# Performance work log

Measured on AMD Instinct MI355X. Metric: run time of the kernel, lower is better.

The kernel has to match this reference:

```python
import jax, jax.numpy as jnp
import numpy as np

EMBED_DIM = 256
N_HEADS = 1
NORM_FACTOR = float(np.sqrt(EMBED_DIM / N_HEADS))


def setup_inputs() -> dict:
    key = jax.random.key(0)
    ks = jax.random.split(key, 7)
    B, S, E = 4, 4096, EMBED_DIM
    scale = 1.0 / np.sqrt(E)
    x = jax.random.normal(ks[0], (B, S, E), dtype=jnp.float32)
    Wq = jax.random.normal(ks[1], (E, E), dtype=jnp.float32) * scale
    bq = jax.random.normal(ks[2], (E,), dtype=jnp.float32) * 0.01
    Wk = jax.random.normal(ks[3], (E, E), dtype=jnp.float32) * scale
    bk = jax.random.normal(ks[4], (E,), dtype=jnp.float32) * 0.01
    Wv = jax.random.normal(ks[5], (E, E), dtype=jnp.float32) * scale
    bv = jax.random.normal(ks[6], (E,), dtype=jnp.float32) * 0.01
    return {"x": x, "Wq": Wq, "bq": bq, "Wk": Wk, "bk": bk, "Wv": Wv, "bv": bv}


def reference(x, Wq, bq, Wk, bk, Wv, bv):
    # Linear projections (torch Linear: x @ W.T + b; W here stored as [in, out]-equivalent square)
    q = x @ Wq + bq  # [B, S, E]
    k = x @ Wk + bk  # [B, S, E]
    v = x @ Wv + bv  # [B, S, E]
    # Full attention scores [B, S, S], scaled by sqrt(embed_dim / n_heads)
    attn_scores = jnp.einsum('bse,bte->bst', q, k) / NORM_FACTOR
    attn_dist = jax.nn.softmax(attn_scores, axis=-1)
    pooled = jnp.einsum('bst,bte->bse', attn_dist, v)  # [B, S, E]
    return pooled.mean(axis=1, keepdims=True)  # [B, 1, E]
```

## Files before the change

### kernel.cpp

```cpp
#include <hip/hip_runtime.h>
#include <hip/hip_fp8.h>
#include <stdint.h>

#define SS 4096
#define EE 256
#define C2 0.0901684400555602f
#define SCALE1 0x7F7F7F7F

typedef __bf16 bf16x8 __attribute__((ext_vector_type(8)));
typedef float  f32x4  __attribute__((ext_vector_type(4)));
typedef int    i32x8  __attribute__((ext_vector_type(8)));

#if __has_builtin(__builtin_amdgcn_exp2f)
#define EXP2(x) __builtin_amdgcn_exp2f(x)
#else
#define EXP2(x) exp2f(x)
#endif
#if __has_builtin(__builtin_amdgcn_rcpf)
#define RCP(x) __builtin_amdgcn_rcpf(x)
#else
#define RCP(x) (1.0f / (x))
#endif

__device__ __forceinline__ uint16_t bf16_rn(float f) {
  uint32_t u = __float_as_uint(f);
  uint32_t r = (u + 0x7fffu + ((u >> 16) & 1u)) >> 16;
  return (uint16_t)r;
}
__device__ __forceinline__ float bf2f(uint16_t h) {
  return __uint_as_float(((uint32_t)h) << 16);
}
__device__ __forceinline__ bf16x8 pack_bf8(float4 a, float4 b) {
  union { bf16x8 v; uint16_t u[8]; } r;
  r.u[0] = bf16_rn(a.x); r.u[1] = bf16_rn(a.y);
  r.u[2] = bf16_rn(a.z); r.u[3] = bf16_rn(a.w);
  r.u[4] = bf16_rn(b.x); r.u[5] = bf16_rn(b.y);
  r.u[6] = bf16_rn(b.z); r.u[7] = bf16_rn(b.w);
  return r.v;
}
__device__ __forceinline__ uint8_t f32_to_e4m3(float x) {
#if __has_builtin(__builtin_amdgcn_cvt_pk_fp8_f32)
  return (uint8_t)(__builtin_amdgcn_cvt_pk_fp8_f32(x, 0.f, 0, false) & 0xff);
#else
  __hip_fp8_e4m3 h(x);
  return (uint8_t)h.__x;
#endif
}

__device__ __forceinline__ f32x4 mfma16(bf16x8 a, bf16x8 b, f32x4 c) {
  return __builtin_amdgcn_mfma_f32_16x16x32_bf16(a, b, c, 0, 0, 0);
}
__device__ __forceinline__ f32x4 mfma128(i32x8 a, i32x8 b, f32x4 c) {
  return __builtin_amdgcn_mfma_scale_f32_16x16x128_f8f6f4(
      a, b, c, 0 , 0 , 0, SCALE1, 0, SCALE1);
}

template<int R>
__device__ __forceinline__ void stage_tile(const uint16_t* gsrc, char* lds, int tid) {
  constexpr int NPER = (R * 32) / 256;
  const int wave = tid >> 6;
  #pragma unroll
  for (int c = 0; c < NPER; ++c) {
    int chunk = c * 256 + tid;
    int r = chunk >> 5;
    int ccl = (chunk & 31) ^ (r & 31);
    const char* gp = (const char*)gsrc + (r * 32 + ccl) * 16;
    char* lp = lds + (c * 256 + wave * 64) * 16;
    __builtin_amdgcn_global_load_lds(
        (const __attribute__((address_space(1))) uint32_t*)(uintptr_t)gp,
        (__attribute__((address_space(3))) uint32_t*)(uintptr_t)lp,
        16, 0, 0);
  }
}
__device__ __forceinline__ bf16x8 read_frag(const char* lds, int row, int cc) {
  int ccp = cc ^ (row & 31);
  return *(const bf16x8*)(lds + (row * 32 + ccp) * 16);
}

__device__ __forceinline__ void stage_fp8_64(const uint8_t* gsrc, char* lds, int tid) {
  #pragma unroll
  for (int c = 0; c < 4; ++c) {
    int chunk = c * 256 + tid;
    int r = chunk >> 4;
    int ccl = (chunk & 15) ^ (r & 15);
    const char* gp = (const char*)gsrc + (r * 16 + ccl) * 16;
    char* lp = lds + (c * 256 + (tid >> 6) * 64) * 16;
    __builtin_amdgcn_global_load_lds(
        (const __attribute__((address_space(1))) uint32_t*)(uintptr_t)gp,
        (__attribute__((address_space(3))) uint32_t*)(uintptr_t)lp,
        16, 0, 0);
  }
}
__device__ __forceinline__ i32x8 read_frag8(const char* lds, int t, int win, int quad) {
  union { i32x8 v; uint4 q[2]; } r;
  int cc0 = win * 8 + quad * 2;
  r.q[0] = *(const uint4*)(lds + (t * 16 + ((cc0 + 0) ^ (t & 15))) * 16);
  r.q[1] = *(const uint4*)(lds + (t * 16 + ((cc0 + 1) ^ (t & 15))) * 16);
  return r.v;
}

__global__ void prep_kernel(const float* __restrict__ Wq, const float* __restrict__ Wk,
                            const float* __restrict__ Wv, uint16_t* __restrict__ wt,
                            float* __restrict__ zbase, float* __restrict__ out) {
  __shared__ float t[64][65];
  const int bid = blockIdx.x, tid = threadIdx.x;
  if (bid >= 48) {
    int idx = (bid - 48) * 256 + tid;
    float4 z = {0.f, 0.f, 0.f, 0.f};
    if (idx < 8192) ((float4*)zbase)[idx] = z;
    else ((float4*)out)[idx - 8192] = z;
    return;
  }
  const int mat = bid >> 4, tt = bid & 15;
  const int ib = (tt >> 2) * 64, ob = (tt & 3) * 64;
  const float* W = (mat == 0) ? Wq : (mat == 1) ? Wk : Wv;
  #pragma unroll
  for (int p = 0; p < 4; ++p) {
    int idx = p * 256 + tid;
    int r = idx >> 4, c4 = idx & 15;
    float4 f = *(const float4*)&W[(size_t)(ib + r) * 256 + ob + c4 * 4];
    t[r][c4 * 4 + 0] = f.x; t[r][c4 * 4 + 1] = f.y;
    t[r][c4 * 4 + 2] = f.z; t[r][c4 * 4 + 3] = f.w;
  }
  __syncthreads();
  #pragma unroll
  for (int p = 0; p < 4; ++p) {
    int idx = p * 256 + tid;
    int o = idx >> 4, i4 = idx & 15;
    ushort4 u;
    u.x = bf16_rn(t[i4 * 4 + 0][o]);
    u.y = bf16_rn(t[i4 * 4 + 1][o]);
    u.z = bf16_rn(t[i4 * 4 + 2][o]);
    u.w = bf16_rn(t[i4 * 4 + 3][o]);
    *(ushort4*)&wt[((size_t)mat * 256 + ob + o) * 256 + ib + i4 * 4] = u;
  }
}

__global__ __launch_bounds__(256, 2) void qkv_kernel(
    const float* __restrict__ x, const uint16_t* __restrict__ wt,
    const float* __restrict__ bq, const float* __restrict__ bk, const float* __restrict__ bv,
    uint8_t* __restrict__ q8, uint8_t* __restrict__ k8, uint16_t* __restrict__ vo) {
  __shared__ char wsm[2][32768];
  const int tid = threadIdx.x;
  const int lane = tid & 63, wave = tid >> 6, quad = lane >> 4, lr = lane & 15;
  const int m0 = (blockIdx.x >> 2) * 128;
  const int cchunk = blockIdx.x & 3;
  stage_tile<64>(wt + (size_t)(cchunk * 192) * 256, wsm[0], tid);
  const float* ab = x + (size_t)(m0 + wave * 32) * EE;
  bf16x8 a[2][8];
  #pragma unroll
  for (int ms = 0; ms < 2; ++ms)
    #pragma unroll
    for (int f = 0; f < 8; ++f) {
      const float* rp = ab + (size_t)(ms * 16 + lr) * EE + f * 32 + quad * 8;
      a[ms][f] = pack_bf8(*(const float4*)rp, *(const float4*)(rp + 4));
    }
  for (int nc = 0; nc < 3; ++nc) {
    __syncthreads();
    if (nc < 2)
      stage_tile<64>(wt + (size_t)(cchunk * 192 + (nc + 1) * 64) * 256, wsm[(nc + 1) & 1], tid);
    const char* tile = wsm[nc & 1];
    #pragma unroll
    for (int nt = 0; nt < 4; ++nt) {
      const int eg0 = cchunk * 192 + nc * 64 + nt * 16;
      const int mat = eg0 >> 8;
      const int e = (eg0 & 255) + lr;
      const float* bias = (mat == 0) ? bq : (mat == 1) ? bk : bv;
      bf16x8 bf[8];
      #pragma unroll
      for (int f = 0; f < 8; ++f) bf[f] = read_frag(tile, nt * 16 + lr, f * 4 + quad);
      f32x4 acc[2] = {};
      #pragma unroll
      for (int f = 0; f < 8; ++f)
        #pragma unroll
        for (int ms = 0; ms < 2; ++ms)
          acc[ms] = mfma16(a[ms][f], bf[f], acc[ms]);
      const float bsv = bias[e];
      #pragma unroll
      for (int ms = 0; ms < 2; ++ms)
        #pragma unroll
        for (int r = 0; r < 4; ++r) {
          int row = m0 + wave * 32 + ms * 16 + quad * 4 + r;
          float vl = acc[ms][r] + bsv;
          if (mat == 2)      vo[(size_t)row * EE + e] = bf16_rn(vl);
          else if (mat == 1) k8[(size_t)row * EE + e] = f32_to_e4m3(vl);
          else               q8[(size_t)row * EE + e] = f32_to_e4m3(vl);
        }
    }
  }
}

__global__ __launch_bounds__(256, 3) void scores_l_kernel(
    const uint8_t* __restrict__ q8, const uint8_t* __restrict__ k8,
    float* __restrict__ lacc) {
  __shared__ char kt[2][16384];
  const int tid = threadIdx.x;
  const int lane = tid & 63, wave = tid >> 6, quad = lane >> 4, lr = lane & 15;
  const int idx = blockIdx.x;
  const int b = idx >> 8, rem = idx & 255, qblk = rem >> 4, kch = rem & 15;
  const uint8_t* qb = q8 + (size_t)(b * SS + qblk * 256 + wave * 64) * EE;
  const uint8_t* kb = k8 + (size_t)(b * SS + kch * 256) * EE;
  stage_fp8_64(kb, kt[0], tid);
  i32x8 a[4][2];
  #pragma unroll
  for (int ms = 0; ms < 4; ++ms)
    #pragma unroll
    for (int win = 0; win < 2; ++win)
      a[ms][win] = *(const i32x8*)(qb + (size_t)(ms * 16 + lr) * EE + win * 128 + quad * 32);
  float accl[16];
  #pragma unroll
  for (int i = 0; i < 16; ++i) accl[i] = 0.f;
  for (int it = 0; it < 4; ++it) {
    __syncthreads();
    if (it + 1 < 4) stage_fp8_64(kb + (size_t)(it + 1) * 64 * EE, kt[(it + 1) & 1], tid);
    const char* tile = kt[it & 1];
    #pragma unroll
    for (int nt = 0; nt < 4; ++nt) {
      i32x8 bf0 = read_frag8(tile, nt * 16 + lr, 0, quad);
      i32x8 bf1 = read_frag8(tile, nt * 16 + lr, 1, quad);
      f32x4 acc[4] = {};
      #pragma unroll
      for (int ms = 0; ms < 4; ++ms) {
        acc[ms] = mfma128(a[ms][0], bf0, acc[ms]);
        acc[ms] = mfma128(a[ms][1], bf1, acc[ms]);
      }
      #pragma unroll
      for (int ms = 0; ms < 4; ++ms)
        #pragma unroll
        for (int r = 0; r < 4; ++r)
          accl[ms * 4 + r] += EXP2(acc[ms][r] * C2);
    }
  }
  #pragma unroll
  for (int d = 1; d < 16; d <<= 1)
    #pragma unroll
    for (int i = 0; i < 16; ++i)
      accl[i] += __shfl_xor(accl[i], d, 64);
  if (lr == 0) {
    float* lp = lacc + b * SS + qblk * 256 + wave * 64;
    #pragma unroll
    for (int ms = 0; ms < 4; ++ms)
      #pragma unroll
      for (int r = 0; r < 4; ++r)
        atomicAdd(&lp[ms * 16 + quad * 4 + r], accl[ms * 4 + r]);
  }
}

__global__ __launch_bounds__(256, 3) void scores_w_kernel(
    const uint8_t* __restrict__ q8, const uint8_t* __restrict__ k8,
    const float* __restrict__ lacc, float* __restrict__ wacc) {
  __shared__ char qt[2][16384];
  __shared__ float rls[256];
  const int tid = threadIdx.x;
  const int lane = tid & 63, wave = tid >> 6, quad = lane >> 4, lr = lane & 15;
  const int idx = blockIdx.x;
  const int b = idx >> 8, rem = idx & 255, kblk = rem >> 4, sch = rem & 15;
  const uint8_t* kb = k8 + (size_t)(b * SS + kblk * 256 + wave * 64) * EE;
  const uint8_t* qw = q8 + (size_t)(b * SS + sch * 256) * EE;
  rls[tid] = lacc[b * SS + sch * 256 + tid];
  stage_fp8_64(qw, qt[0], tid);
  i32x8 a[4][2];
  #pragma unroll
  for (int ms = 0; ms < 4; ++ms)
    #pragma unroll
    for (int win = 0; win < 2; ++win)
      a[ms][win] = *(const i32x8*)(kb + (size_t)(ms * 16 + lr) * EE + win * 128 + quad * 32);
  float accw[16];
  #pragma unroll
  for (int i = 0; i < 16; ++i) accw[i] = 0.f;
  for (int it = 0; it < 4; ++it) {
    __syncthreads();
    if (it + 1 < 4) stage_fp8_64(qw + (size_t)(it + 1) * 64 * EE, qt[(it + 1) & 1], tid);
    const char* tile = qt[it & 1];
    #pragma unroll
    for (int nt = 0; nt < 4; ++nt) {
      float rlv = RCP(rls[it * 64 + nt * 16 + lr]);
      i32x8 bf0 = read_frag8(tile, nt * 16 + lr, 0, quad);
      i32x8 bf1 = read_frag8(tile, nt * 16 + lr, 1, quad);
      f32x4 acc[4] = {};
      #pragma unroll
      for (int ms = 0; ms < 4; ++ms) {
        acc[ms] = mfma128(a[ms][0], bf0, acc[ms]);
        acc[ms] = mfma128(a[ms][1], bf1, acc[ms]);
      }
      #pragma unroll
      for (int ms = 0; ms < 4; ++ms)
        #pragma unroll
        for (int r = 0; r < 4; ++r)
          accw[ms * 4 + r] += EXP2(acc[ms][r] * C2) * rlv;
    }
  }
  #pragma unroll
  for (int d = 1; d < 16; d <<= 1)
    #pragma unroll
    for (int i = 0; i < 16; ++i)
      accw[i] += __shfl_xor(accw[i], d, 64);
  if (lr == 0) {
    float* wp = wacc + b * SS + kblk * 256 + wave * 64;
    #pragma unroll
    for (int ms = 0; ms < 4; ++ms)
      #pragma unroll
      for (int r = 0; r < 4; ++r)
        atomicAdd(&wp[ms * 16 + quad * 4 + r], accw[ms * 4 + r]);
  }
}

__global__ void pool_kernel(const float* __restrict__ wsum, const uint16_t* __restrict__ v,
                            float* __restrict__ out) {
  __shared__ float red[4][256];
  const int b = blockIdx.x >> 6, tc = blockIdx.x & 63;
  const int tq = threadIdx.x >> 6, eg = threadIdx.x & 63;
  float acc[4] = {0.f, 0.f, 0.f, 0.f};
  const float* wp = wsum + b * SS + tc * 64;
  const uint16_t* vp = v + (size_t)(b * SS + tc * 64) * EE + eg * 4;
  #pragma unroll
  for (int t = 0; t < 16; ++t) {
    int row = t * 4 + tq;
    float wv = wp[row];
    ushort4 x4 = *(const ushort4*)(vp + (size_t)row * EE);
    acc[0] += wv * bf2f(x4.x);
    acc[1] += wv * bf2f(x4.y);
    acc[2] += wv * bf2f(x4.z);
    acc[3] += wv * bf2f(x4.w);
  }
  #pragma unroll
  for (int j = 0; j < 4; ++j) red[tq][eg * 4 + j] = acc[j];
  __syncthreads();
  if (tq == 0) {
    const float inv = 1.0f / 4096.0f;
    #pragma unroll
    for (int j = 0; j < 4; ++j) {
      float s = red[0][eg * 4 + j] + red[1][eg * 4 + j] +
                red[2][eg * 4 + j] + red[3][eg * 4 + j];
      atomicAdd(&out[b * 256 + eg * 4 + j], s * inv);
    }
  }
}

extern "C" void kernel_launch(void* const* d_in, const int* in_sizes, int n_in,
                              void* d_out, int out_size, void* d_ws, size_t ws_size,
                              hipStream_t stream) {
  const float* x  = (const float*)d_in[0];
  const float* Wq = (const float*)d_in[1];
  const float* bq = (const float*)d_in[2];
  const float* Wk = (const float*)d_in[3];
  const float* bk = (const float*)d_in[4];
  const float* Wv = (const float*)d_in[5];
  const float* bv = (const float*)d_in[6];

  char* ws = (char*)d_ws;
  uint8_t*  q8   = (uint8_t*)(ws);
  uint8_t*  k8   = (uint8_t*)(ws + 4194304);
  uint16_t* vb   = (uint16_t*)(ws + 8388608);
  uint16_t* wt   = (uint16_t*)(ws + 16777216);
  float* l_arr   = (float*)(ws + 17170432);
  float* w_arr   = (float*)(ws + 17235968);
  float* out     = (float*)d_out;

  prep_kernel<<<81, 256, 0, stream>>>(Wq, Wk, Wv, wt, l_arr, out);
  qkv_kernel<<<512, 256, 0, stream>>>(x, wt, bq, bk, bv, q8, k8, vb);
  scores_l_kernel<<<1024, 256, 0, stream>>>(q8, k8, l_arr);
  scores_w_kernel<<<1024, 256, 0, stream>>>(q8, k8, l_arr, w_arr);
  pool_kernel<<<256, 256, 0, stream>>>(w_arr, vb, out);
}
```

Baseline: 153.7 us.

## Materialize fp8 exp scores once instead of recomputing QK^T in two passes

Replaces the two score passes (one building row sums l, one recomputing QK^T to build column weights) with a single pass. That pass computes exp scores, stores them as an fp8 matrix (64 MB), and accumulates row sums. A new wsum kernel then streams the fp8 matrix, scales each row by 1/l and reduces into per-block partials, which pool_kernel sums. This removes one full fp8 GEMM-plus-exp pass but adds a large HBM write and read, and it clamps exponents at ZMAX, which changes the numerics.

```diff
diff --git a/kernel.cpp b/kernel.cpp
--- a/kernel.cpp
+++ b/kernel.cpp
@@ -6,9 +6,11 @@
 #define EE 256
 #define C2 0.0901684400555602f
 #define SCALE1 0x7F7F7F7F
+#define ZMAX 8.5f
 
 typedef __bf16 bf16x8 __attribute__((ext_vector_type(8)));
 typedef float  f32x4  __attribute__((ext_vector_type(4)));
+typedef float  f32x2  __attribute__((ext_vector_type(2)));
 typedef int    i32x8  __attribute__((ext_vector_type(8)));
 
 #if __has_builtin(__builtin_amdgcn_exp2f)
@@ -44,6 +46,33 @@
 #else
   __hip_fp8_e4m3 h(x);
   return (uint8_t)h.__x;
+#endif
+}
+__device__ __forceinline__ uint32_t pack4_e4m3(float a, float b, float c, float d) {
+#if __has_builtin(__builtin_amdgcn_cvt_pk_fp8_f32)
+  int v = __builtin_amdgcn_cvt_pk_fp8_f32(a, b, 0, false);
+  v = __builtin_amdgcn_cvt_pk_fp8_f32(c, d, v, true);
+  return (uint32_t)v;
+#else
+  return (uint32_t)f32_to_e4m3(a) | ((uint32_t)f32_to_e4m3(b) << 8) |
+         ((uint32_t)f32_to_e4m3(c) << 16) | ((uint32_t)f32_to_e4m3(d) << 24);
+#endif
+}
+__device__ __forceinline__ float e4m3_f32(uint32_t u) {
+  uint32_t bits = ((u & 0x80u) << 24) | ((u & 0x7fu) << 20);
+  return __uint_as_float(bits) * 0x1p+120f;
+}
+__device__ __forceinline__ void decode_fma4(uint32_t w, float rv, float* acc) {
+#if __has_builtin(__builtin_amdgcn_cvt_pk_f32_fp8)
+  f32x2 lo = __builtin_amdgcn_cvt_pk_f32_fp8((int)w, false);
+  f32x2 hi = __builtin_amdgcn_cvt_pk_f32_fp8((int)w, true);
+  acc[0] += rv * lo[0]; acc[1] += rv * lo[1];
+  acc[2] += rv * hi[0]; acc[3] += rv * hi[1];
+#else
+  acc[0] += rv * e4m3_f32(w & 0xffu);
+  acc[1] += rv * e4m3_f32((w >> 8) & 0xffu);
+  acc[2] += rv * e4m3_f32((w >> 16) & 0xffu);
+  acc[3] += rv * e4m3_f32(w >> 24);
 #endif
 }
 
@@ -190,74 +219,18 @@
   }
 }
 
-__global__ __launch_bounds__(256, 3) void scores_l_kernel(
+__global__ __launch_bounds__(256, 3) void scores_pl_kernel(
     const uint8_t* __restrict__ q8, const uint8_t* __restrict__ k8,
-    float* __restrict__ lacc) {
-  __shared__ char kt[2][16384];
-  const int tid = threadIdx.x;
-  const int lane = tid & 63, wave = tid >> 6, quad = lane >> 4, lr = lane & 15;
-  const int idx = blockIdx.x;
-  const int b = idx >> 8, rem = idx & 255, qblk = rem >> 4, kch = rem & 15;
-  const uint8_t* qb = q8 + (size_t)(b * SS + qblk * 256 + wave * 64) * EE;
-  const uint8_t* kb = k8 + (size_t)(b * SS + kch * 256) * EE;
-  stage_fp8_64(kb, kt[0], tid);
-  i32x8 a[4][2];
-  #pragma unroll
-  for (int ms = 0; ms < 4; ++ms)
-    #pragma unroll
-    for (int win = 0; win < 2; ++win)
-      a[ms][win] = *(const i32x8*)(qb + (size_t)(ms * 16 + lr) * EE + win * 128 + quad * 32);
-  float accl[16];
-  #pragma unroll
-  for (int i = 0; i < 16; ++i) accl[i] = 0.f;
-  for (int it = 0; it < 4; ++it) {
-    __syncthreads();
-    if (it + 1 < 4) stage_fp8_64(kb + (size_t)(it + 1) * 64 * EE, kt[(it + 1) & 1], tid);
-    const char* tile = kt[it & 1];
-    #pragma unroll
-    for (int nt = 0; nt < 4; ++nt) {
-      i32x8 bf0 = read_frag8(tile, nt * 16 + lr, 0, quad);
-      i32x8 bf1 = read_frag8(tile, nt * 16 + lr, 1, quad);
-      f32x4 acc[4] = {};
-      #pragma unroll
-      for (int ms = 0; ms < 4; ++ms) {
-        acc[ms] = mfma128(a[ms][0], bf0, acc[ms]);
-        acc[ms] = mfma128(a[ms][1], bf1, acc[ms]);
-      }
-      #pragma unroll
-      for (int ms = 0; ms < 4; ++ms)
-        #pragma unroll
-        for (int r = 0; r < 4; ++r)
-          accl[ms * 4 + r] += EXP2(acc[ms][r] * C2);
-    }
-  }
-  #pragma unroll
-  for (int d = 1; d < 16; d <<= 1)
-    #pragma unroll
-    for (int i = 0; i < 16; ++i)
-      accl[i] += __shfl_xor(accl[i], d, 64);
-  if (lr == 0) {
-    float* lp = lacc + b * SS + qblk * 256 + wave * 64;
-    #pragma unroll
-    for (int ms = 0; ms < 4; ++ms)
-      #pragma unroll
-      for (int r = 0; r < 4; ++r)
-        atomicAdd(&lp[ms * 16 + quad * 4 + r], accl[ms * 4 + r]);
-  }
-}
-
-__global__ __launch_bounds__(256, 3) void scores_w_kernel(
-    const uint8_t* __restrict__ q8, const uint8_t* __restrict__ k8,
-    const float* __restrict__ lacc, float* __restrict__ wacc) {
+    uint8_t* __restrict__ p8, float* __restrict__ lacc) {
   __shared__ char qt[2][16384];
-  __shared__ float rls[256];
+  __shared__ float lsh[256];
   const int tid = threadIdx.x;
   const int lane = tid & 63, wave = tid >> 6, quad = lane >> 4, lr = lane & 15;
   const int idx = blockIdx.x;
   const int b = idx >> 8, rem = idx & 255, kblk = rem >> 4, sch = rem & 15;
   const uint8_t* kb = k8 + (size_t)(b * SS + kblk * 256 + wave * 64) * EE;
   const uint8_t* qw = q8 + (size_t)(b * SS + sch * 256) * EE;
-  rls[tid] = lacc[b * SS + sch * 256 + tid];
+  lsh[tid] = 0.f;
   stage_fp8_64(qw, qt[0], tid);
   i32x8 a[4][2];
   #pragma unroll
@@ -265,16 +238,13 @@
     #pragma unroll
     for (int win = 0; win < 2; ++win)
       a[ms][win] = *(const i32x8*)(kb + (size_t)(ms * 16 + lr) * EE + win * 128 + quad * 32);
-  float accw[16];
-  #pragma unroll
-  for (int i = 0; i < 16; ++i) accw[i] = 0.f;
+  const int tcol0 = kblk * 256 + wave * 64 + quad * 4;
   for (int it = 0; it < 4; ++it) {
     __syncthreads();
     if (it + 1 < 4) stage_fp8_64(qw + (size_t)(it + 1) * 64 * EE, qt[(it + 1) & 1], tid);
     const char* tile = qt[it & 1];
     #pragma unroll
     for (int nt = 0; nt < 4; ++nt) {
-      float rlv = RCP(rls[it * 64 + nt * 16 + lr]);
       i32x8 bf0 = read_frag8(tile, nt * 16 + lr, 0, quad);
       i32x8 bf1 = read_frag8(tile, nt * 16 + lr, 1, quad);
       f32x4 acc[4] = {};
@@ -283,40 +253,79 @@
         acc[ms] = mfma128(a[ms][0], bf0, acc[ms]);
         acc[ms] = mfma128(a[ms][1], bf1, acc[ms]);
       }
-      #pragma unroll
-      for (int ms = 0; ms < 4; ++ms)
-        #pragma unroll
-        for (int r = 0; r < 4; ++r)
-          accw[ms * 4 + r] += EXP2(acc[ms][r] * C2) * rlv;
+      const int sloc = it * 64 + nt * 16 + lr;
+      uint8_t* pr = p8 + (((size_t)(b * SS + sch * 256 + sloc)) << 12) + tcol0;
+      float lpart = 0.f;
+      #pragma unroll
+      for (int ms = 0; ms < 4; ++ms) {
+        float e0 = EXP2(fminf(acc[ms][0] * C2, ZMAX));
+        float e1 = EXP2(fminf(acc[ms][1] * C2, ZMAX));
+        float e2 = EXP2(fminf(acc[ms][2] * C2, ZMAX));
+        float e3 = EXP2(fminf(acc[ms][3] * C2, ZMAX));
+        lpart += (e0 + e1) + (e2 + e3);
+        *(uint32_t*)(pr + ms * 16) = pack4_e4m3(e0, e1, e2, e3);
+      }
+      lpart += __shfl_xor(lpart, 16, 64);
+      lpart += __shfl_xor(lpart, 32, 64);
+      if (quad == 0) atomicAdd(&lsh[sloc], lpart);
     }
   }
-  #pragma unroll
-  for (int d = 1; d < 16; d <<= 1)
-    #pragma unroll
-    for (int i = 0; i < 16; ++i)
-      accw[i] += __shfl_xor(accw[i], d, 64);
-  if (lr == 0) {
-    float* wp = wacc + b * SS + kblk * 256 + wave * 64;
-    #pragma unroll
-    for (int ms = 0; ms < 4; ++ms)
-      #pragma unroll
-      for (int r = 0; r < 4; ++r)
-        atomicAdd(&wp[ms * 16 + quad * 4 + r], accw[ms * 4 + r]);
-  }
-}
-
-__global__ void pool_kernel(const float* __restrict__ wsum, const uint16_t* __restrict__ v,
+  __syncthreads();
+  atomicAdd(&lacc[b * SS + sch * 256 + tid], lsh[tid]);
+}
+
+__global__ __launch_bounds__(256) void wsum_kernel(
+    const uint8_t* __restrict__ p8, const float* __restrict__ lacc,
+    float* __restrict__ wpart) {
+  __shared__ float rls[64];
+  const int tid = threadIdx.x;
+  const int b = blockIdx.x >> 6, sb = blockIdx.x & 63;
+  if (tid < 64) rls[tid] = RCP(lacc[b * SS + sb * 64 + tid]);
+  __syncthreads();
+  const uint8_t* pp = p8 + (((size_t)(b * SS + sb * 64)) << 12) + tid * 16;
+  float acc[16];
+  #pragma unroll
+  for (int i = 0; i < 16; ++i) acc[i] = 0.f;
+  #pragma unroll 8
+  for (int s = 0; s < 64; ++s) {
+    uint4 pv = *(const uint4*)(pp + ((size_t)s << 12));
+    float rv = rls[s];
+    decode_fma4(pv.x, rv, acc + 0);
+    decode_fma4(pv.y, rv, acc + 4);
+    decode_fma4(pv.z, rv, acc + 8);
+    decode_fma4(pv.w, rv, acc + 12);
+  }
+  float* wp = wpart + (((size_t)(b * 64 + sb)) << 12) + tid * 16;
+  #pragma unroll
+  for (int i = 0; i < 4; ++i)
+    *(float4*)(wp + i * 4) =
+        make_float4(acc[i * 4], acc[i * 4 + 1], acc[i * 4 + 2], acc[i * 4 + 3]);
+}
+
+__global__ void pool_kernel(const float* __restrict__ wpart, const uint16_t* __restrict__ v,
                             float* __restrict__ out) {
   __shared__ float red[4][256];
+  __shared__ float wred[4][64];
+  __shared__ float wl[64];
   const int b = blockIdx.x >> 6, tc = blockIdx.x & 63;
-  const int tq = threadIdx.x >> 6, eg = threadIdx.x & 63;
+  const int tid = threadIdx.x;
+  const int tq = tid >> 6, eg = tid & 63;
+  {
+    float p = 0.f;
+    const float* wq = wpart + (((size_t)(b * 64 + tq * 16)) << 12) + tc * 64 + eg;
+    #pragma unroll
+    for (int j = 0; j < 16; ++j) p += wq[(size_t)j << 12];
+    wred[tq][eg] = p;
+  }
+  __syncthreads();
+  if (tid < 64) wl[tid] = wred[0][tid] + wred[1][tid] + wred[2][tid] + wred[3][tid];
+  __syncthreads();
   float acc[4] = {0.f, 0.f, 0.f, 0.f};
-  const float* wp = wsum + b * SS + tc * 64;
   const uint16_t* vp = v + (size_t)(b * SS + tc * 64) * EE + eg * 4;
   #pragma unroll
   for (int t = 0; t < 16; ++t) {
     int row = t * 4 + tq;
-    float wv = wp[row];
+    float wv = wl[row];
     ushort4 x4 = *(const ushort4*)(vp + (size_t)row * EE);
     acc[0] += wv * bf2f(x4.x);
     acc[1] += wv * bf2f(x4.y);
@@ -349,17 +358,18 @@
   const float* bv = (const float*)d_in[6];
 
   char* ws = (char*)d_ws;
-  uint8_t*  q8   = (uint8_t*)(ws);
-  uint8_t*  k8   = (uint8_t*)(ws + 4194304);
-  uint16_t* vb   = (uint16_t*)(ws + 8388608);
-  uint16_t* wt   = (uint16_t*)(ws + 16777216);
-  float* l_arr   = (float*)(ws + 17170432);
-  float* w_arr   = (float*)(ws + 17235968);
-  float* out     = (float*)d_out;
+  uint8_t*  q8    = (uint8_t*)(ws);
+  uint8_t*  k8    = (uint8_t*)(ws + 4194304);
+  uint16_t* vb    = (uint16_t*)(ws + 8388608);
+  uint16_t* wt    = (uint16_t*)(ws + 16777216);
+  float*    l_arr = (float*)(ws + 17170432);
+  float*    wpart = (float*)(ws + 20971520);
+  uint8_t*  p8    = (uint8_t*)(ws + 33554432);
+  float* out      = (float*)d_out;
 
   prep_kernel<<<81, 256, 0, stream>>>(Wq, Wk, Wv, wt, l_arr, out);
   qkv_kernel<<<512, 256, 0, stream>>>(x, wt, bq, bk, bv, q8, k8, vb);
-  scores_l_kernel<<<1024, 256, 0, stream>>>(q8, k8, l_arr);
-  scores_w_kernel<<<1024, 256, 0, stream>>>(q8, k8, l_arr, w_arr);
-  pool_kernel<<<256, 256, 0, stream>>>(w_arr, vb, out);
-}
+  scores_pl_kernel<<<1024, 256, 0, stream>>>(q8, k8, p8, l_arr);
+  wsum_kernel<<<256, 256, 0, stream>>>(p8, l_arr, wpart);
+  pool_kernel<<<256, 256, 0, stream>>>(wpart, vb, out);
+}
```

After: 161.0 us. 1.05x slower.
